# Performance work log

Hardware: AMD Instinct MI355X
Metric: run time of the kernel (lower is better)

The kernel has to match this reference:

```python
import jax, jax.numpy as jnp
import numpy as np

B, S, E = 2, 2048, 1024
HID = 1024
HEADS = 16
EPS = 1e-5
SCALE = (E * 2) ** (-0.5)  # source uses input_data_dim*2


def setup_inputs() -> dict:
    key = jax.random.key(0)
    k1, k2, k3 = jax.random.split(key, 3)
    return {
        "x": jax.random.normal(k1, (B, S, E), dtype=jnp.float32),
        "ln_g": jnp.ones((E,), jnp.float32),
        "ln_b": jnp.zeros((E,), jnp.float32),
        "W1": jax.random.normal(k2, (E, 3 * HID), jnp.float32) * 0.02,
        "b1": jnp.zeros((3 * HID,), jnp.float32),
        "W2": jax.random.normal(k3, (HID, HID), jnp.float32) * 0.02,
        "b2": jnp.zeros((HID,), jnp.float32),
    }


def reference(x, ln_g, ln_b, W1, b1, W2, b2):
    # LayerNorm over last dim
    mu = jnp.mean(x, axis=-1, keepdims=True)
    var = jnp.mean(jnp.square(x - mu), axis=-1, keepdims=True)
    xn = (x - mu) * jax.lax.rsqrt(var + EPS) * ln_g + ln_b
    # QKV projection: [B,S,3*HID]
    qkv = jnp.einsum('bse,ef->bsf', xn, W1) + b1
    # Faithful to source: flat reshape to (heads, B, S, 3*HID/heads)
    qkv_heads = qkv.reshape(HEADS, B, S, -1)
    q, k, v = jnp.split(qkv_heads, 3, axis=-1)  # each [H,B,S,d]
    scores = jnp.einsum('hbse,hbSe->hbsS', q, k) * SCALE  # [H,B,S,S]
    att = jax.nn.softmax(scores, axis=-1)
    full_att = jnp.einsum('hbsS,hbSe->hbse', att, v)  # [H,B,S,d]
    full_att = full_att.reshape(B, S, -1)  # faithful flat reshape -> [B,S,HID]
    out = jnp.einsum('bsh,hk->bsk', full_att, W2) + b2
    return out
```

## Files before the change

### kernel.cpp

```cpp
#include <hip/hip_runtime.h>

typedef unsigned short u16;
typedef __bf16 bf16x8 __attribute__((ext_vector_type(8)));
typedef float f32x4 __attribute__((ext_vector_type(4)));
typedef float f32x16 __attribute__((ext_vector_type(16)));
typedef unsigned int u32x4 __attribute__((ext_vector_type(4)));
typedef int i32x2 __attribute__((ext_vector_type(2)));

static constexpr float SCALE2 = 0.022097086912079608f * 1.4426950408889634f;

__device__ __forceinline__ u16 f2b(float f) {
  union { float f; unsigned int i; } v; v.f = f;
  unsigned int r = v.i + 0x7fffu + ((v.i >> 16) & 1u);
  return (u16)(r >> 16);
}
__device__ __forceinline__ unsigned int pk2(float a, float b) {
#if __has_builtin(__builtin_amdgcn_cvt_pk_bf16_f32)
  auto v = __builtin_amdgcn_cvt_pk_bf16_f32(a, b);
  unsigned int u;
  __builtin_memcpy(&u, &v, 4);
  return u;
#else
  union { float f; unsigned int i; } x, y; x.f = a; y.f = b;
  return ((x.i + 0x8000u) >> 16) | ((y.i + 0x8000u) & 0xffff0000u);
#endif
}
__device__ __forceinline__ i32x2 plswap(unsigned int a, unsigned int b) {
#if __has_builtin(__builtin_amdgcn_permlane32_swap)
  return __builtin_amdgcn_permlane32_swap((int)a, (int)b, false, false);
#else
  int d = (int)a, s = (int)b;
  asm volatile("v_permlane32_swap_b32 %0, %1" : "+v"(d), "+v"(s));
  i32x2 r; r[0] = d; r[1] = s; return r;
#endif
}
__device__ __forceinline__ void async16(const u16* g, u16* l) {
  __builtin_amdgcn_global_load_lds((const __attribute__((address_space(1))) void*)g,
                                   (__attribute__((address_space(3))) void*)l,
                                   16, 0, 0);
}

__global__ __launch_bounds__(256) void pre_kernel(const float* __restrict__ x,
                                                  const float* __restrict__ lg,
                                                  const float* __restrict__ lb,
                                                  u16* __restrict__ xn,
                                                  const float* __restrict__ W1,
                                                  u16* __restrict__ W1T,
                                                  const float* __restrict__ W2,
                                                  u16* __restrict__ W2T) {
  __shared__ __align__(16) u16 smem[64 * 72];
  const int bx = blockIdx.x;
  const int t = threadIdx.x;
  if (bx < 4096) {
    float* red = (float*)smem;
    const int row = bx;
    float4 v = *(const float4*)(x + (size_t)row * 1024 + t * 4);
    float s = v.x + v.y + v.z + v.w;
    float ss = v.x * v.x + v.y * v.y + v.z * v.z + v.w * v.w;
    for (int off = 32; off >= 1; off >>= 1) {
      s += __shfl_xor(s, off, 64);
      ss += __shfl_xor(ss, off, 64);
    }
    const int w = t >> 6;
    if ((t & 63) == 0) { red[w] = s; red[4 + w] = ss; }
    __syncthreads();
    s = red[0] + red[1] + red[2] + red[3];
    ss = red[4] + red[5] + red[6] + red[7];
    const float mu = s * (1.0f / 1024.0f);
    const float var = ss * (1.0f / 1024.0f) - mu * mu;
    const float inv = rsqrtf(var + 1e-5f);
    float4 gg = *(const float4*)(lg + t * 4);
    float4 bb = *(const float4*)(lb + t * 4);
    ushort4 o;
    o.x = f2b((v.x - mu) * inv * gg.x + bb.x);
    o.y = f2b((v.y - mu) * inv * gg.y + bb.y);
    o.z = f2b((v.z - mu) * inv * gg.z + bb.z);
    o.w = f2b((v.w - mu) * inv * gg.w + bb.w);
    *(ushort4*)(xn + (size_t)row * 1024 + t * 4) = o;
    return;
  }
  const float* in;
  u16* out;
  int C, c0, r0;
  if (bx < 4096 + 768) {
    const int idx = bx - 4096;
    C = 3072; in = W1; out = W1T;
    c0 = (idx % 48) * 64; r0 = (idx / 48) * 64;
  } else {
    const int idx = bx - 4864;
    C = 1024; in = W2; out = W2T;
    c0 = (idx % 16) * 64; r0 = (idx / 16) * 64;
  }
  const int row = t >> 2, cseg = t & 3;
  for (int it = 0; it < 4; it++) {
    float4 v = *(const float4*)&in[(size_t)(r0 + row) * C + c0 + it * 16 + cseg * 4];
    ushort4 o;
    o.x = f2b(v.x); o.y = f2b(v.y); o.z = f2b(v.z); o.w = f2b(v.w);
    *(ushort4*)&smem[row * 72 + it * 16 + cseg * 4] = o;
  }
  __syncthreads();
  const int orow = t >> 2, ch = t & 3;
  u16 vals[16];
  for (int j = 0; j < 16; j++) vals[j] = smem[(ch * 16 + j) * 72 + orow];
  u16* dp = out + (size_t)(c0 + orow) * 1024 + r0 + ch * 16;
  *(uint4*)&dp[0] = *(uint4*)&vals[0];
  *(uint4*)&dp[8] = *(uint4*)&vals[8];
}

template <int MODE, int MT>
__global__ __launch_bounds__(256) void gemm_bt(const u16* __restrict__ A,
                                               const u16* __restrict__ Bt,
                                               const float* __restrict__ bias,
                                               float* __restrict__ C,
                                               int M, int N, int K,
                                               u16* __restrict__ Qc,
                                               u16* __restrict__ Kc,
                                               u16* __restrict__ Vtmp) {
  __shared__ __align__(16) u16 SMEM[8192];
  u16* As = SMEM;
  u16* Bs = SMEM + MT * 32;
  const int m0 = blockIdx.y * MT, n0 = blockIdx.x * 128;
  const int t = threadIdx.x, w = t >> 6, lane = t & 63;
  const int q = lane >> 4, l16 = lane & 15;
  const int wm = (w >> 1) * (MT / 2), wn = (w & 1) * 64;
  constexpr int NI = MT / 32;

  const int sc = (lane & 3) ^ ((lane >> 3) & 3);
  const u16* ap = A + (size_t)(m0 + w * 16 + (lane >> 2)) * K + sc * 8;
  const u16* bp = Bt + (size_t)(n0 + w * 16 + (lane >> 2)) * K + sc * 8;
  u16* lA = &As[w * 512];
  u16* lB = &Bs[w * 512];
  const int ac = q ^ ((l16 >> 1) & 3);

  f32x4 acc[NI][4];
  const f32x4 zero = {0.f, 0.f, 0.f, 0.f};
  for (int i = 0; i < NI; i++)
    for (int j = 0; j < 4; j++) acc[i][j] = zero;

  for (int k0 = 0; k0 < K; k0 += 32) {
    for (int i = 0; i < MT / 64; i++)
      async16(ap + (size_t)(i * 64) * K, lA + i * 2048);
    for (int i = 0; i < 2; i++)
      async16(bp + (size_t)(i * 64) * K, lB + i * 2048);
    ap += 32; bp += 32;
    __syncthreads();
    bf16x8 af[NI], bfr[4];
    for (int i = 0; i < NI; i++)
      af[i] = *(const bf16x8*)&As[(wm + i * 16 + l16) * 32 + ac * 8];
    for (int j = 0; j < 4; j++)
      bfr[j] = *(const bf16x8*)&Bs[(wn + j * 16 + l16) * 32 + ac * 8];
    for (int i = 0; i < NI; i++)
      for (int j = 0; j < 4; j++)
        acc[i][j] = __builtin_amdgcn_mfma_f32_16x16x32_bf16(af[i], bfr[j], acc[i][j], 0, 0, 0);
    __syncthreads();
  }

  if constexpr (MODE == 0) {
    for (int j = 0; j < 4; j++) {
      const int col = n0 + wn + j * 16 + l16;
      const float bv = bias[col];
      for (int i = 0; i < NI; i++) {
        const int rbase = m0 + wm + i * 16 + q * 4;
        for (int r = 0; r < 4; r++)
          C[(size_t)(rbase + r) * N + col] = acc[i][j][r] + bv;
      }
    }
  } else {
    const int seg = n0 + wn;
    const int k64 = seg >> 6;
    const int tcol = k64 / 3;
    const int typ = k64 - tcol * 3;
    u16* dst = (typ == 0) ? Qc : (typ == 1) ? Kc : Vtmp;
    const float qs = (typ == 0) ? SCALE2 : 1.0f;
    const int gidx = m0 >> 7;
    u16* tw = &SMEM[w * 1280];
    float bv[4];
    for (int j = 0; j < 4; j++) bv[j] = bias[seg + j * 16 + l16];
    __syncthreads();
    for (int i = 0; i < 4; i++) {
      for (int j = 0; j < 4; j++) {
        ushort4 pk;
        pk.x = f2b((acc[i][j][0] + bv[j]) * qs);
        pk.y = f2b((acc[i][j][1] + bv[j]) * qs);
        pk.z = f2b((acc[i][j][2] + bv[j]) * qs);
        pk.w = f2b((acc[i][j][3] + bv[j]) * qs);
        *(ushort4*)&tw[(j * 16 + l16) * 20 + q * 4] = pk;
      }
      const int r2 = lane >> 2;
      const int quarter = lane & 3;
      u16 vals[16];
      for (int c = 0; c < 16; c++)
        vals[c] = tw[(quarter * 16 + c) * 20 + r2];
      const int lr = wm + i * 16 + r2;
      const int s = (lr << 4) + tcol;
      u16* dp = dst + ((size_t)gidx * 2048 + s) * 64 + quarter * 16;
      *(uint4*)&dp[0] = *(uint4*)&vals[0];
      *(uint4*)&dp[8] = *(uint4*)&vals[8];
    }
  }
}

__global__ __launch_bounds__(256) void vtrans(const u16* __restrict__ Vtmp,
                                              u16* __restrict__ Vt) {
  __shared__ __align__(16) u16 tile[64 * 64];
  const int g = blockIdx.y, s0 = blockIdx.x * 64;
  const int t = threadIdx.x;
  const int row = t >> 3, ch = t & 7;
  for (int p = 0; p < 2; p++) {
    const int r = p * 32 + row;
    uint4 v = *(const uint4*)&Vtmp[((size_t)g * 2048 + s0 + r) * 64 + ch * 8];
    *(uint4*)&tile[r * 64 + ((ch ^ (r & 7)) * 8)] = v;
  }
  __syncthreads();
  const int d = t >> 2, scn = t & 3;
  u16 vals[16];
  for (int j2 = 0; j2 < 16; j2++) {
    const int s = scn * 16 + j2;
    vals[j2] = tile[s * 64 + (((d >> 3) ^ (s & 7)) * 8) + (d & 7)];
  }
  u16* dp = Vt + ((size_t)g * 64 + d) * 2048 + s0 + scn * 16;
  *(uint4*)&dp[0] = *(uint4*)&vals[0];
  *(uint4*)&dp[8] = *(uint4*)&vals[8];
}

__global__ __launch_bounds__(512) void attn_kernel(const u16* __restrict__ Qc,
                                                   const u16* __restrict__ Kc,
                                                   const u16* __restrict__ Vt,
                                                   u16* __restrict__ Oc) {
  __shared__ __align__(16) u16 LDS[25600];
  u16* K0 = LDS;
  u16* K1 = LDS + 4096;
  u16* V0 = LDS + 8192;
  u16* V1 = LDS + 12288;
  const int g = blockIdx.y;
  const int q0 = blockIdx.x * 128;
  const int t = threadIdx.x, w = t >> 6, lane = t & 63;
  const int l31 = lane & 31, h = lane >> 5;
  const int qs = w & 3;
  const int kvb = (w >> 2) * 32;

  const u16* Qg = Qc + (size_t)g * 2048 * 64;
  const u16* Kg = Kc + (size_t)g * 2048 * 64;
  const u16* Vg = Vt + (size_t)g * 64 * 2048;

  bf16x8 aq[4];
#pragma unroll
  for (int s = 0; s < 4; s++)
    aq[s] = *(const bf16x8*)&Qg[(size_t)(q0 + qs * 32 + l31) * 64 + s * 16 + h * 8];

  f32x16 accO[2];
#pragma unroll
  for (int tt = 0; tt < 2; tt++)
#pragma unroll
    for (int r = 0; r < 16; r++) accO[tt][r] = 0.f;
  float psv = 0.f;

  const int ch = (lane & 7) ^ ((lane >> 3) & 7);
  const u16* kp = Kg + (size_t)(w * 8 + (lane >> 3)) * 64 + ch * 8;
  const u16* vp = Vg + (size_t)(w * 8 + (lane >> 3)) * 2048 + ch * 8;
  u16* lK0 = K0 + w * 512;
  u16* lK1 = K1 + w * 512;
  u16* lV0 = V0 + w * 512;
  u16* lV1 = V1 + w * 512;

  const int rsw = l31 & 7;

  async16(kp, lK0);
  async16(vp, lV0);
  __syncthreads();

  for (int it = 0; it < 32; it++) {
    const int cur = it & 1;
    const u16* Kcur = cur ? K1 : K0;
    const u16* Vcur = cur ? V1 : V0;
    if (it < 31) {
      const int kt0 = (it + 1) * 64;
      async16(kp + (size_t)kt0 * 64, cur ? lK0 : lK1);
      async16(vp + kt0, cur ? lV0 : lV1);
    }

    f32x16 sa;
#pragma unroll
    for (int r = 0; r < 16; r++) sa[r] = 0.f;
    __builtin_amdgcn_s_setprio(1);
#pragma unroll
    for (int s = 0; s < 4; s++) {
      bf16x8 ak = *(const bf16x8*)&Kcur[(kvb + l31) * 64 + (((s * 2 + h) ^ rsw) * 8)];
      sa = __builtin_amdgcn_mfma_f32_32x32x16_bf16(ak, aq[s], sa, 0, 0, 0);
    }
    __builtin_amdgcn_s_setprio(0);

    float e[16];
#pragma unroll
    for (int r = 0; r < 16; r++) e[r] = __builtin_amdgcn_exp2f(sa[r]);
    psv += (((e[0] + e[1]) + (e[2] + e[3])) + ((e[4] + e[5]) + (e[6] + e[7])))
         + (((e[8] + e[9]) + (e[10] + e[11])) + ((e[12] + e[13]) + (e[14] + e[15])));
    unsigned int c[8];
#pragma unroll
    for (int m = 0; m < 8; m++) c[m] = pk2(e[2 * m], e[2 * m + 1]);
    i32x2 r02 = plswap(c[0], c[2]);
    i32x2 r13 = plswap(c[1], c[3]);
    i32x2 r46 = plswap(c[4], c[6]);
    i32x2 r57 = plswap(c[5], c[7]);
    bf16x8 pf[2];
    u32x4 f0 = {(unsigned)r02[0], (unsigned)r13[0], (unsigned)r02[1], (unsigned)r13[1]};
    u32x4 f1 = {(unsigned)r46[0], (unsigned)r57[0], (unsigned)r46[1], (unsigned)r57[1]};
    __builtin_memcpy(&pf[0], &f0, 16);
    __builtin_memcpy(&pf[1], &f1, 16);

    __builtin_amdgcn_s_setprio(1);
#pragma unroll
    for (int s = 0; s < 2; s++) {
#pragma unroll
      for (int tt = 0; tt < 2; tt++) {
        bf16x8 av = *(const bf16x8*)&Vcur[(tt * 32 + l31) * 64 + ((((kvb >> 3) + s * 2 + h) ^ rsw) * 8)];
        accO[tt] = __builtin_amdgcn_mfma_f32_32x32x16_bf16(av, pf[s], accO[tt], 0, 0, 0);
      }
    }
    __builtin_amdgcn_s_setprio(0);

    __syncthreads();
  }

  float* Red = (float*)LDS;
  if (w >= 4) {
    const int base = (w - 4) * 2048;
#pragma unroll
    for (int tt = 0; tt < 2; tt++)
#pragma unroll
      for (int m = 0; m < 4; m++) {
        f32x4 v4 = {accO[tt][4 * m], accO[tt][4 * m + 1], accO[tt][4 * m + 2], accO[tt][4 * m + 3]};
        *(f32x4*)&Red[base + (tt * 4 + m) * 256 + lane * 4] = v4;
      }
    Red[8192 + (w - 4) * 64 + lane] = psv;
  }
  __syncthreads();
  if (w < 4) {
#pragma unroll
    for (int tt = 0; tt < 2; tt++)
#pragma unroll
      for (int m = 0; m < 4; m++) {
        f32x4 v4 = *(const f32x4*)&Red[w * 2048 + (tt * 4 + m) * 256 + lane * 4];
        accO[tt][4 * m + 0] += v4[0];
        accO[tt][4 * m + 1] += v4[1];
        accO[tt][4 * m + 2] += v4[2];
        accO[tt][4 * m + 3] += v4[3];
      }
    psv += Red[8192 + w * 64 + lane];
    psv += __shfl_xor(psv, 32, 64);
    const float linv = 1.0f / psv;
    const int srow = q0 + qs * 32 + l31;
    const int orow = g * 128 + (srow >> 4);
    const int cbase = (srow & 15) * 64;
#pragma unroll
    for (int tt = 0; tt < 2; tt++)
#pragma unroll
      for (int m = 0; m < 4; m++) {
        ushort4 o;
        o.x = f2b(accO[tt][4 * m + 0] * linv);
        o.y = f2b(accO[tt][4 * m + 1] * linv);
        o.z = f2b(accO[tt][4 * m + 2] * linv);
        o.w = f2b(accO[tt][4 * m + 3] * linv);
        *(ushort4*)&Oc[(size_t)orow * 1024 + cbase + tt * 32 + m * 8 + h * 4] = o;
      }
  }
}

extern "C" void kernel_launch(void* const* d_in, const int* in_sizes, int n_in,
                              void* d_out, int out_size, void* d_ws, size_t ws_size,
                              hipStream_t stream) {
  (void)in_sizes; (void)n_in; (void)out_size; (void)ws_size;
  const float* x    = (const float*)d_in[0];
  const float* ln_g = (const float*)d_in[1];
  const float* ln_b = (const float*)d_in[2];
  const float* W1   = (const float*)d_in[3];
  const float* b1   = (const float*)d_in[4];
  const float* W2   = (const float*)d_in[5];
  const float* b2   = (const float*)d_in[6];

  char* ws = (char*)d_ws;
  u16* xn   = (u16*)(ws);
  u16* W1T  = (u16*)(ws + ((size_t)8 << 20));
  u16* W2T  = (u16*)(ws + ((size_t)14 << 20));
  u16* Qc   = (u16*)(ws + ((size_t)16 << 20));
  u16* Kc   = (u16*)(ws + ((size_t)24 << 20));
  u16* Vtmp = (u16*)(ws + ((size_t)32 << 20));
  u16* Vt   = (u16*)(ws + ((size_t)40 << 20));
  u16* Oc   = xn;

  pre_kernel<<<dim3(5120), dim3(256), 0, stream>>>(x, ln_g, ln_b, xn, W1, W1T, W2, W2T);
  gemm_bt<1, 128><<<dim3(24, 32), dim3(256), 0, stream>>>(xn, W1T, b1, nullptr,
                                                          4096, 3072, 1024, Qc, Kc, Vtmp);
  vtrans<<<dim3(32, 32), dim3(256), 0, stream>>>(Vtmp, Vt);
  attn_kernel<<<dim3(16, 32), dim3(512), 0, stream>>>(Qc, Kc, Vt, Oc);
  gemm_bt<0, 64><<<dim3(8, 64), dim3(256), 0, stream>>>(Oc, W2T, b2, (float*)d_out,
                                                        4096, 1024, 1024, nullptr, nullptr, nullptr);
}
```

Baseline: 195.2 us.

## Triple-buffer K/V tiles with explicit vmcnt waits and one barrier per iteration

Replaces the double-buffered K/V prefetch in the attention loop with a three-stage ring buffer that prefetches two tiles ahead. Each iteration waits with s_waitcnt vmcnt on only the oldest outstanding loads before a raw s_barrier, instead of using a full __syncthreads that drains every load. The aim is to keep more global-to-LDS traffic in flight and hide load latency behind the MFMA work. It uses more of the already-allocated LDS and relies on hand-counted vmcnt values, which break if the async load count per stage changes.

```diff
diff --git a/kernel.cpp b/kernel.cpp
--- a/kernel.cpp
+++ b/kernel.cpp
@@ -228,10 +228,6 @@
                                                    const u16* __restrict__ Vt,
                                                    u16* __restrict__ Oc) {
   __shared__ __align__(16) u16 LDS[25600];
-  u16* K0 = LDS;
-  u16* K1 = LDS + 4096;
-  u16* V0 = LDS + 8192;
-  u16* V1 = LDS + 12288;
   const int g = blockIdx.y;
   const int q0 = blockIdx.x * 128;
   const int t = threadIdx.x, w = t >> 6, lane = t & 63;
@@ -258,25 +254,31 @@
   const int ch = (lane & 7) ^ ((lane >> 3) & 7);
   const u16* kp = Kg + (size_t)(w * 8 + (lane >> 3)) * 64 + ch * 8;
   const u16* vp = Vg + (size_t)(w * 8 + (lane >> 3)) * 2048 + ch * 8;
-  u16* lK0 = K0 + w * 512;
-  u16* lK1 = K1 + w * 512;
-  u16* lV0 = V0 + w * 512;
-  u16* lV1 = V1 + w * 512;
+  const int so = w * 512;
+
+  u16* B0k = LDS;          u16* B1k = LDS + 4096;   u16* B2k = LDS + 8192;
+  u16* B0v = LDS + 12288;  u16* B1v = LDS + 16384;  u16* B2v = LDS + 20480;
 
   const int rsw = l31 & 7;
 
-  async16(kp, lK0);
-  async16(vp, lV0);
-  __syncthreads();
+  async16(kp, B0k + so);
+  async16(vp, B0v + so);
+  async16(kp + 4096, B1k + so);
+  async16(vp + 64, B1v + so);
+
+  u16 *rK0 = B0k, *rK1 = B1k, *rK2 = B2k;
+  u16 *rV0 = B0v, *rV1 = B1v, *rV2 = B2v;
 
   for (int it = 0; it < 32; it++) {
-    const int cur = it & 1;
-    const u16* Kcur = cur ? K1 : K0;
-    const u16* Vcur = cur ? V1 : V0;
-    if (it < 31) {
-      const int kt0 = (it + 1) * 64;
-      async16(kp + (size_t)kt0 * 64, cur ? lK0 : lK1);
-      async16(vp + kt0, cur ? lV0 : lV1);
+    if (it < 31) asm volatile("s_waitcnt vmcnt(2)" ::: "memory");
+    else         asm volatile("s_waitcnt vmcnt(0)" ::: "memory");
+    __builtin_amdgcn_sched_barrier(0);
+    __builtin_amdgcn_s_barrier();
+    __builtin_amdgcn_sched_barrier(0);
+    if (it < 30) {
+      const int kt0 = (it + 2) * 64;
+      async16(kp + (size_t)kt0 * 64, rK2 + so);
+      async16(vp + kt0, rV2 + so);
     }
 
     f32x16 sa;
@@ -285,7 +287,7 @@
     __builtin_amdgcn_s_setprio(1);
 #pragma unroll
     for (int s = 0; s < 4; s++) {
-      bf16x8 ak = *(const bf16x8*)&Kcur[(kvb + l31) * 64 + (((s * 2 + h) ^ rsw) * 8)];
+      bf16x8 ak = *(const bf16x8*)&rK0[(kvb + l31) * 64 + (((s * 2 + h) ^ rsw) * 8)];
       sa = __builtin_amdgcn_mfma_f32_32x32x16_bf16(ak, aq[s], sa, 0, 0, 0);
     }
     __builtin_amdgcn_s_setprio(0);
@@ -313,14 +315,17 @@
     for (int s = 0; s < 2; s++) {
 #pragma unroll
       for (int tt = 0; tt < 2; tt++) {
-        bf16x8 av = *(const bf16x8*)&Vcur[(tt * 32 + l31) * 64 + ((((kvb >> 3) + s * 2 + h) ^ rsw) * 8)];
+        bf16x8 av = *(const bf16x8*)&rV0[(tt * 32 + l31) * 64 + ((((kvb >> 3) + s * 2 + h) ^ rsw) * 8)];
         accO[tt] = __builtin_amdgcn_mfma_f32_32x32x16_bf16(av, pf[s], accO[tt], 0, 0, 0);
       }
     }
     __builtin_amdgcn_s_setprio(0);
 
-    __syncthreads();
-  }
+    u16* tk = rK0; rK0 = rK1; rK1 = rK2; rK2 = tk;
+    u16* tv = rV0; rV0 = rV1; rV1 = rV2; rV2 = tv;
+  }
+
+  __syncthreads();
 
   float* Red = (float*)LDS;
   if (w >= 4) {
```

Measured after the change: 194.7 us. Within noise of the previous version (-0.3%).

## Double attention block to 16 waves with four-way KV split and tree reduction

Applied to the files above, without the earlier changes.

The attention kernel grows from 512 to 1024 threads, so each block processes 128-key tiles per iteration with four KV-quarter wave groups instead of two, halving the loop trip count. K/V staging buffers double in LDS size, and the V load swizzle is adapted to 128-wide rows. The final cross-wave partial-sum reduction becomes a two-stage tree with an extra barrier. The goal is more parallelism per query tile and fewer synchronised iterations, at the cost of larger LDS, register pressure from launch_bounds(1024), and extra reduction steps.

```diff
diff --git a/kernel.cpp b/kernel.cpp
--- a/kernel.cpp
+++ b/kernel.cpp
@@ -223,21 +223,21 @@
   *(uint4*)&dp[8] = *(uint4*)&vals[8];
 }
 
-__global__ __launch_bounds__(512) void attn_kernel(const u16* __restrict__ Qc,
-                                                   const u16* __restrict__ Kc,
-                                                   const u16* __restrict__ Vt,
-                                                   u16* __restrict__ Oc) {
-  __shared__ __align__(16) u16 LDS[25600];
+__global__ __launch_bounds__(1024, 8) void attn_kernel(const u16* __restrict__ Qc,
+                                                       const u16* __restrict__ Kc,
+                                                       const u16* __restrict__ Vt,
+                                                       u16* __restrict__ Oc) {
+  __shared__ __align__(16) u16 LDS[33792];
   u16* K0 = LDS;
-  u16* K1 = LDS + 4096;
-  u16* V0 = LDS + 8192;
-  u16* V1 = LDS + 12288;
+  u16* K1 = LDS + 8192;
+  u16* V0 = LDS + 16384;
+  u16* V1 = LDS + 24576;
   const int g = blockIdx.y;
   const int q0 = blockIdx.x * 128;
   const int t = threadIdx.x, w = t >> 6, lane = t & 63;
   const int l31 = lane & 31, h = lane >> 5;
   const int qs = w & 3;
-  const int kvb = (w >> 2) * 32;
+  const int kvq = w >> 2;
 
   const u16* Qg = Qc + (size_t)g * 2048 * 64;
   const u16* Kg = Kc + (size_t)g * 2048 * 64;
@@ -255,28 +255,26 @@
     for (int r = 0; r < 16; r++) accO[tt][r] = 0.f;
   float psv = 0.f;
 
-  const int ch = (lane & 7) ^ ((lane >> 3) & 7);
-  const u16* kp = Kg + (size_t)(w * 8 + (lane >> 3)) * 64 + ch * 8;
-  const u16* vp = Vg + (size_t)(w * 8 + (lane >> 3)) * 2048 + ch * 8;
-  u16* lK0 = K0 + w * 512;
-  u16* lK1 = K1 + w * 512;
-  u16* lV0 = V0 + w * 512;
-  u16* lV1 = V1 + w * 512;
+  const int kc = (lane & 7) ^ ((lane >> 3) & 7);
+  const int vc = (lane & 15) ^ ((w * 4 + (lane >> 4)) & 7);
+  const u16* kp = Kg + (size_t)(w * 8 + (lane >> 3)) * 64 + kc * 8;
+  const u16* vp = Vg + (size_t)(w * 4 + (lane >> 4)) * 2048 + vc * 8;
+  const int so = w * 512;
 
   const int rsw = l31 & 7;
 
-  async16(kp, lK0);
-  async16(vp, lV0);
-  __syncthreads();
-
-  for (int it = 0; it < 32; it++) {
+  async16(kp, K0 + so);
+  async16(vp, V0 + so);
+  __syncthreads();
+
+  for (int it = 0; it < 16; it++) {
     const int cur = it & 1;
     const u16* Kcur = cur ? K1 : K0;
     const u16* Vcur = cur ? V1 : V0;
-    if (it < 31) {
-      const int kt0 = (it + 1) * 64;
-      async16(kp + (size_t)kt0 * 64, cur ? lK0 : lK1);
-      async16(vp + kt0, cur ? lV0 : lV1);
+    if (it < 15) {
+      const int kt0 = (it + 1) * 128;
+      async16(kp + (size_t)kt0 * 64, (cur ? K0 : K1) + so);
+      async16(vp + kt0, (cur ? V0 : V1) + so);
     }
 
     f32x16 sa;
@@ -285,7 +283,7 @@
     __builtin_amdgcn_s_setprio(1);
 #pragma unroll
     for (int s = 0; s < 4; s++) {
-      bf16x8 ak = *(const bf16x8*)&Kcur[(kvb + l31) * 64 + (((s * 2 + h) ^ rsw) * 8)];
+      bf16x8 ak = *(const bf16x8*)&Kcur[(kvq * 32 + l31) * 64 + (((s * 2 + h) ^ rsw) * 8)];
       sa = __builtin_amdgcn_mfma_f32_32x32x16_bf16(ak, aq[s], sa, 0, 0, 0);
     }
     __builtin_amdgcn_s_setprio(0);
@@ -313,7 +311,7 @@
     for (int s = 0; s < 2; s++) {
 #pragma unroll
       for (int tt = 0; tt < 2; tt++) {
-        bf16x8 av = *(const bf16x8*)&Vcur[(tt * 32 + l31) * 64 + ((((kvb >> 3) + s * 2 + h) ^ rsw) * 8)];
+        bf16x8 av = *(const bf16x8*)&Vcur[(tt * 32 + l31) * 128 + (((kvq * 4 + s * 2 + h) ^ rsw) * 8)];
         accO[tt] = __builtin_amdgcn_mfma_f32_32x32x16_bf16(av, pf[s], accO[tt], 0, 0, 0);
       }
     }
@@ -323,30 +321,59 @@
   }
 
   float* Red = (float*)LDS;
-  if (w >= 4) {
-    const int base = (w - 4) * 2048;
+  float* Psum = Red + 16384;
+  if (kvq >= 2) {
+    const int reg = (w - 8) * 2048;
 #pragma unroll
     for (int tt = 0; tt < 2; tt++)
 #pragma unroll
       for (int m = 0; m < 4; m++) {
         f32x4 v4 = {accO[tt][4 * m], accO[tt][4 * m + 1], accO[tt][4 * m + 2], accO[tt][4 * m + 3]};
-        *(f32x4*)&Red[base + (tt * 4 + m) * 256 + lane * 4] = v4;
-      }
-    Red[8192 + (w - 4) * 64 + lane] = psv;
-  }
-  __syncthreads();
-  if (w < 4) {
+        *(f32x4*)&Red[reg + (tt * 4 + m) * 256 + lane * 4] = v4;
+      }
+    Psum[(w - 8) * 64 + lane] = psv;
+  }
+  __syncthreads();
+  if (kvq < 2) {
+    const int reg = w * 2048;
 #pragma unroll
     for (int tt = 0; tt < 2; tt++)
 #pragma unroll
       for (int m = 0; m < 4; m++) {
-        f32x4 v4 = *(const f32x4*)&Red[w * 2048 + (tt * 4 + m) * 256 + lane * 4];
+        f32x4 v4 = *(const f32x4*)&Red[reg + (tt * 4 + m) * 256 + lane * 4];
         accO[tt][4 * m + 0] += v4[0];
         accO[tt][4 * m + 1] += v4[1];
         accO[tt][4 * m + 2] += v4[2];
         accO[tt][4 * m + 3] += v4[3];
       }
-    psv += Red[8192 + w * 64 + lane];
+    psv += Psum[w * 64 + lane];
+  }
+  __syncthreads();
+  if (kvq == 1) {
+    const int reg = (w - 4) * 2048;
+#pragma unroll
+    for (int tt = 0; tt < 2; tt++)
+#pragma unroll
+      for (int m = 0; m < 4; m++) {
+        f32x4 v4 = {accO[tt][4 * m], accO[tt][4 * m + 1], accO[tt][4 * m + 2], accO[tt][4 * m + 3]};
+        *(f32x4*)&Red[reg + (tt * 4 + m) * 256 + lane * 4] = v4;
+      }
+    Psum[(w - 4) * 64 + lane] = psv;
+  }
+  __syncthreads();
+  if (kvq == 0) {
+    const int reg = w * 2048;
+#pragma unroll
+    for (int tt = 0; tt < 2; tt++)
+#pragma unroll
+      for (int m = 0; m < 4; m++) {
+        f32x4 v4 = *(const f32x4*)&Red[reg + (tt * 4 + m) * 256 + lane * 4];
+        accO[tt][4 * m + 0] += v4[0];
+        accO[tt][4 * m + 1] += v4[1];
+        accO[tt][4 * m + 2] += v4[2];
+        accO[tt][4 * m + 3] += v4[3];
+      }
+    psv += Psum[w * 64 + lane];
     psv += __shfl_xor(psv, 32, 64);
     const float linv = 1.0f / psv;
     const int srow = q0 + qs * 32 + l31;
@@ -392,7 +419,7 @@
   gemm_bt<1, 128><<<dim3(24, 32), dim3(256), 0, stream>>>(xn, W1T, b1, nullptr,
                                                           4096, 3072, 1024, Qc, Kc, Vtmp);
   vtrans<<<dim3(32, 32), dim3(256), 0, stream>>>(Vtmp, Vt);
-  attn_kernel<<<dim3(16, 32), dim3(512), 0, stream>>>(Qc, Kc, Vt, Oc);
+  attn_kernel<<<dim3(16, 32), dim3(1024), 0, stream>>>(Qc, Kc, Vt, Oc);
   gemm_bt<0, 64><<<dim3(8, 64), dim3(256), 0, stream>>>(Oc, W2T, b2, (float*)d_out,
                                                         4096, 1024, 1024, nullptr, nullptr, nullptr);
 }
```

After: 506.6 us. +159.6%, slower.

## Double GEMM K-tile to 64 with XOR-8 swizzle and XCD-aware block remap

Applied to the files above, without the earlier changes.

The GEMM main loop now stages 64-wide K slices instead of 32, halving the number of barrier pairs per tile, and uses an 8-way XOR chunk swizzle in LDS to keep the fragment reads free of bank conflicts. The grid is flattened to 1D and block IDs are remapped so consecutive tiles go to the same XCD (assuming 8 XCDs), improving L2 reuse of A/B panels. LDS use doubles (up to 32KB for MT=128), which may lower occupancy.

```diff
diff --git a/kernel.cpp b/kernel.cpp
--- a/kernel.cpp
+++ b/kernel.cpp
@@ -112,46 +112,55 @@
                                                const u16* __restrict__ Bt,
                                                const float* __restrict__ bias,
                                                float* __restrict__ C,
-                                               int M, int N, int K,
+                                               int M, int N, int K, int nbx,
                                                u16* __restrict__ Qc,
                                                u16* __restrict__ Kc,
                                                u16* __restrict__ Vtmp) {
-  __shared__ __align__(16) u16 SMEM[8192];
+  __shared__ __align__(16) u16 SMEM[(MT + 128) * 64];
   u16* As = SMEM;
-  u16* Bs = SMEM + MT * 32;
-  const int m0 = blockIdx.y * MT, n0 = blockIdx.x * 128;
+  u16* Bs = SMEM + MT * 64;
+  const int nwg = gridDim.x, cpx = nwg >> 3;
+  const int l0 = blockIdx.x;
+  const int l2 = (l0 & 7) * cpx + (l0 >> 3);
+  const int bx = l2 % nbx, by = l2 / nbx;
+  const int m0 = by * MT, n0 = bx * 128;
   const int t = threadIdx.x, w = t >> 6, lane = t & 63;
   const int q = lane >> 4, l16 = lane & 15;
   const int wm = (w >> 1) * (MT / 2), wn = (w & 1) * 64;
   constexpr int NI = MT / 32;
 
-  const int sc = (lane & 3) ^ ((lane >> 3) & 3);
-  const u16* ap = A + (size_t)(m0 + w * 16 + (lane >> 2)) * K + sc * 8;
-  const u16* bp = Bt + (size_t)(n0 + w * 16 + (lane >> 2)) * K + sc * 8;
+  const int gchunk = (lane & 7) ^ ((lane >> 3) & 7);
+  const u16* ap = A + (size_t)(m0 + w * 8 + (lane >> 3)) * K + gchunk * 8;
+  const u16* bp = Bt + (size_t)(n0 + w * 8 + (lane >> 3)) * K + gchunk * 8;
   u16* lA = &As[w * 512];
   u16* lB = &Bs[w * 512];
-  const int ac = q ^ ((l16 >> 1) & 3);
 
   f32x4 acc[NI][4];
   const f32x4 zero = {0.f, 0.f, 0.f, 0.f};
   for (int i = 0; i < NI; i++)
     for (int j = 0; j < 4; j++) acc[i][j] = zero;
 
-  for (int k0 = 0; k0 < K; k0 += 32) {
-    for (int i = 0; i < MT / 64; i++)
-      async16(ap + (size_t)(i * 64) * K, lA + i * 2048);
-    for (int i = 0; i < 2; i++)
-      async16(bp + (size_t)(i * 64) * K, lB + i * 2048);
-    ap += 32; bp += 32;
+  for (int k0 = 0; k0 < K; k0 += 64) {
+    for (int i = 0; i < MT / 32; i++)
+      async16(ap + (size_t)(i * 32) * K, lA + i * 2048);
+    for (int i = 0; i < 4; i++)
+      async16(bp + (size_t)(i * 32) * K, lB + i * 2048);
+    ap += 64; bp += 64;
     __syncthreads();
-    bf16x8 af[NI], bfr[4];
-    for (int i = 0; i < NI; i++)
-      af[i] = *(const bf16x8*)&As[(wm + i * 16 + l16) * 32 + ac * 8];
-    for (int j = 0; j < 4; j++)
-      bfr[j] = *(const bf16x8*)&Bs[(wn + j * 16 + l16) * 32 + ac * 8];
-    for (int i = 0; i < NI; i++)
-      for (int j = 0; j < 4; j++)
-        acc[i][j] = __builtin_amdgcn_mfma_f32_16x16x32_bf16(af[i], bfr[j], acc[i][j], 0, 0, 0);
+    for (int kk = 0; kk < 2; kk++) {
+      bf16x8 af[NI], bfr[4];
+      for (int i = 0; i < NI; i++) {
+        const int r = wm + i * 16 + l16;
+        af[i] = *(const bf16x8*)&As[r * 64 + (((kk * 4 + q) ^ (r & 7)) * 8)];
+      }
+      for (int j = 0; j < 4; j++) {
+        const int r = wn + j * 16 + l16;
+        bfr[j] = *(const bf16x8*)&Bs[r * 64 + (((kk * 4 + q) ^ (r & 7)) * 8)];
+      }
+      for (int i = 0; i < NI; i++)
+        for (int j = 0; j < 4; j++)
+          acc[i][j] = __builtin_amdgcn_mfma_f32_16x16x32_bf16(af[i], bfr[j], acc[i][j], 0, 0, 0);
+    }
     __syncthreads();
   }
 
@@ -389,10 +398,10 @@
   u16* Oc   = xn;
 
   pre_kernel<<<dim3(5120), dim3(256), 0, stream>>>(x, ln_g, ln_b, xn, W1, W1T, W2, W2T);
-  gemm_bt<1, 128><<<dim3(24, 32), dim3(256), 0, stream>>>(xn, W1T, b1, nullptr,
-                                                          4096, 3072, 1024, Qc, Kc, Vtmp);
+  gemm_bt<1, 128><<<dim3(768), dim3(256), 0, stream>>>(xn, W1T, b1, nullptr,
+                                                       4096, 3072, 1024, 24, Qc, Kc, Vtmp);
   vtrans<<<dim3(32, 32), dim3(256), 0, stream>>>(Vtmp, Vt);
   attn_kernel<<<dim3(16, 32), dim3(512), 0, stream>>>(Qc, Kc, Vt, Oc);
-  gemm_bt<0, 64><<<dim3(8, 64), dim3(256), 0, stream>>>(Oc, W2T, b2, (float*)d_out,
-                                                        4096, 1024, 1024, nullptr, nullptr, nullptr);
-}
+  gemm_bt<0, 64><<<dim3(512), dim3(256), 0, stream>>>(Oc, W2T, b2, (float*)d_out,
+                                                      4096, 1024, 1024, 8, nullptr, nullptr, nullptr);
+}
```

Result: faster. 187.2 us (-4.1%).
